# Performance work log

Measured on AMD Instinct MI355X. Metric: run time of the kernel, lower is better.

Reference implementation:

```python
import jax, jax.numpy as jnp
import numpy as np

EPS = 1e-5

def _layernorm(x, w, b):
    mu = jnp.mean(x, axis=-1, keepdims=True)
    var = jnp.mean(jnp.square(x - mu), axis=-1, keepdims=True)
    return (x - mu) * jax.lax.rsqrt(var + EPS) * w + b

def setup_inputs() -> dict:
    key = jax.random.key(0)
    ks = jax.random.split(key, 8)
    B, N, C, D = 32, 1024, 4096, 64
    x = jax.random.normal(ks[0], (B, N, C), dtype=jnp.float32)
    gumbel = jax.random.gumbel(ks[1], (B, N, 2), dtype=jnp.float32)
    ln_w = jnp.ones((C,), jnp.float32)
    ln_b = jnp.zeros((C,), jnp.float32)
    w1 = jax.random.normal(ks[2], (C, D), dtype=jnp.float32) * 0.02
    b1 = jnp.zeros((D,), jnp.float32)
    w2 = jax.random.normal(ks[3], (D, 2), dtype=jnp.float32) * 0.02
    b2 = jnp.zeros((2,), jnp.float32)
    return {"x": x, "gumbel": gumbel, "ln_w": ln_w, "ln_b": ln_b,
            "w1": w1, "b1": b1, "w2": w2, "b2": b2}

def reference(x, gumbel, ln_w, ln_b, w1, b1, w2, b2):
    B, N, C = x.shape
    xn = _layernorm(x, ln_w, ln_b)
    local_x = xn[:, :, : C // 2]                      # [B, N, C/2]
    # policy is all-ones -> weighted mean over tokens
    global_x = jnp.mean(xn[:, :, C // 2:], axis=1, keepdims=True)  # [B, 1, C/2]
    feat = jnp.concatenate(
        [local_x, jnp.broadcast_to(global_x, local_x.shape)], axis=-1)  # [B, N, C]
    h = jax.nn.gelu(feat @ w1 + b1, approximate=False)  # [B, N, 64]
    logits = h @ w2 + b2                                # [B, N, 2]
    pred_score = jax.nn.log_softmax(logits, axis=-1)
    # gumbel-softmax (tau=1, hard=True) with straight-through estimator
    y_soft = jax.nn.softmax(pred_score + gumbel, axis=-1)
    hard = jax.nn.one_hot(jnp.argmax(y_soft, axis=-1), 2, dtype=y_soft.dtype)
    y = hard - jax.lax.stop_gradient(y_soft) + y_soft
    keep = y[:, :, 0]                                   # [B, N]
    # dense equivalent of masked_select/split: zero out dropped tokens
    return x * keep[:, :, None]
```

## Files before the change

kernel.cpp:

```cpp
#include <hip/hip_runtime.h>
#include <math.h>

#define B_   32
#define N_   1024
#define C_   4096
#define HC_  2048
#define D_   64
#define NT_  32768
#define BKC_ 128
#define NCH_ (HC_ / BKC_)
#define AST_ 68

__device__ __forceinline__ float4 ld4(const float* p) {
    return *reinterpret_cast<const float4*>(p);
}

__global__ __launch_bounds__(256) void mk1(
        const float* __restrict__ x, const float* __restrict__ lnw,
        const float* __restrict__ lnb, const float* __restrict__ w1,
        float* __restrict__ Pp, float* __restrict__ muv,
        float* __restrict__ rsv, float* __restrict__ part) {
    __shared__ float smem[16896];
    __shared__ float sLow[64], qLow[64];
    float* As = smem;
    float* Bsm = smem + 8704;

    const int t = threadIdx.x;
    const int tid = blockIdx.x;
    const int T0 = tid * 64;
    const int row = t >> 2;
    const int fq = t & 3;
    const int lane = t & 63, w = t >> 6;
    const int rt = lane >> 3, dt = lane & 7;

    float acc[64];
#pragma unroll
    for (int i = 0; i < 64; ++i) acc[i] = 0.f;
    float sR = 0.f, qR = 0.f;

    float4 xv[8];
    float4 wv[8];
    float lw[8];
    {
        const float* rp = x + (size_t)(T0 + row) * C_ + fq * 32;
#pragma unroll
        for (int i = 0; i < 8; ++i) xv[i] = ld4(rp + i * 4);
        const float4* s4 = reinterpret_cast<const float4*>(w1);
#pragma unroll
        for (int i = 0; i < 8; ++i) {
            wv[i] = s4[i * 256 + t];
            lw[i] = lnw[(i * 256 + t) >> 4];
        }
    }

#pragma unroll 1
    for (int c = 0; c < NCH_; ++c) {
#pragma unroll
        for (int i = 0; i < 8; ++i) {
            const float4 v = xv[i];
            const int kl = fq * 32 + i * 4;
            As[(kl + 0) * AST_ + row] = v.x;
            As[(kl + 1) * AST_ + row] = v.y;
            As[(kl + 2) * AST_ + row] = v.z;
            As[(kl + 3) * AST_ + row] = v.w;
            sR += (v.x + v.y) + (v.z + v.w);
            qR = fmaf(v.x, v.x, fmaf(v.y, v.y,
                 fmaf(v.z, v.z, fmaf(v.w, v.w, qR))));
        }
        {
            float4* b4 = reinterpret_cast<float4*>(Bsm);
#pragma unroll
            for (int i = 0; i < 8; ++i) {
                float4 v = wv[i];
                v.x *= lw[i]; v.y *= lw[i]; v.z *= lw[i]; v.w *= lw[i];
                b4[i * 256 + t] = v;
            }
        }
        __syncthreads();
        if (c + 1 < NCH_) {
            const int k1 = (c + 1) * BKC_;
            const float* rp = x + (size_t)(T0 + row) * C_ + k1 + fq * 32;
#pragma unroll
            for (int i = 0; i < 8; ++i) xv[i] = ld4(rp + i * 4);
            const float4* s4 = reinterpret_cast<const float4*>(
                w1 + (size_t)k1 * D_);
#pragma unroll
            for (int i = 0; i < 8; ++i) {
                wv[i] = s4[i * 256 + t];
                lw[i] = lnw[k1 + ((i * 256 + t) >> 4)];
            }
        }
#pragma unroll 8
        for (int kk = 0; kk < 32; ++kk) {
            const int k = w * 32 + kk;
            const float4 a0 = *reinterpret_cast<const float4*>(
                As + k * AST_ + rt * 8);
            const float4 a1 = *reinterpret_cast<const float4*>(
                As + k * AST_ + rt * 8 + 4);
            const float4 b0 = *reinterpret_cast<const float4*>(
                Bsm + k * 64 + dt * 8);
            const float4 b1 = *reinterpret_cast<const float4*>(
                Bsm + k * 64 + dt * 8 + 4);
            const float av[8] = {a0.x, a0.y, a0.z, a0.w,
                                 a1.x, a1.y, a1.z, a1.w};
            const float bv[8] = {b0.x, b0.y, b0.z, b0.w,
                                 b1.x, b1.y, b1.z, b1.w};
#pragma unroll
            for (int ri = 0; ri < 8; ++ri)
#pragma unroll
                for (int cj = 0; cj < 8; ++cj)
                    acc[ri * 8 + cj] =
                        fmaf(av[ri], bv[cj], acc[ri * 8 + cj]);
        }
        __syncthreads();
    }
    sR += __shfl_xor(sR, 1); qR += __shfl_xor(qR, 1);
    sR += __shfl_xor(sR, 2); qR += __shfl_xor(qR, 2);
    if (fq == 0) { sLow[row] = sR; qLow[row] = qR; }

#pragma unroll
    for (int i = 0; i < 64; ++i) smem[i * 256 + t] = acc[i];
    __syncthreads();
#pragma unroll
    for (int r2 = 0; r2 < 2; ++r2) {
        const int rowO = rt * 8 + w * 2 + r2;
        float v[8];
#pragma unroll
        for (int cj = 0; cj < 8; ++cj) {
            const int i = w * 16 + r2 * 8 + cj;
            v[cj] = (smem[i * 256 + lane]
                     + smem[i * 256 + 64 + lane])
                  + (smem[i * 256 + 128 + lane]
                     + smem[i * 256 + 192 + lane]);
        }
        float* dst = Pp + (size_t)(T0 + rowO) * D_ + dt * 8;
        *reinterpret_cast<float4*>(dst) =
            make_float4(v[0], v[1], v[2], v[3]);
        *reinterpret_cast<float4*>(dst + 4) =
            make_float4(v[4], v[5], v[6], v[7]);
    }
    __syncthreads();

    float4 wvu[8], bvu[8], gacc[8];
#pragma unroll
    for (int m = 0; m < 8; ++m) {
        wvu[m] = ld4(lnw + HC_ + (m * 64 + lane) * 4);
        bvu[m] = ld4(lnb + HC_ + (m * 64 + lane) * 4);
        gacc[m] = make_float4(0.f, 0.f, 0.f, 0.f);
    }
    for (int i = 0; i < 16; ++i) {
        const int r = w * 16 + i;
        const int tok = T0 + r;
        const float* rowp = x + (size_t)tok * C_ + HC_;
        float4 v[8];
        float s = 0.f, q = 0.f;
#pragma unroll
        for (int m = 0; m < 8; ++m) {
            v[m] = ld4(rowp + (m * 64 + lane) * 4);
            s += (v[m].x + v[m].y) + (v[m].z + v[m].w);
            q = fmaf(v[m].x, v[m].x, fmaf(v[m].y, v[m].y,
                fmaf(v[m].z, v[m].z, fmaf(v[m].w, v[m].w, q))));
        }
#pragma unroll
        for (int o = 1; o < 64; o <<= 1) {
            s += __shfl_xor(s, o);
            q += __shfl_xor(q, o);
        }
        const float S_ = s + sLow[r];
        const float Q_ = q + qLow[r];
        const float mu = S_ * (1.f / C_);
        const float rs = rsqrtf(Q_ * (1.f / C_) - mu * mu + 1e-5f);
        if (lane == 0) {
            muv[tok] = mu;
            rsv[tok] = rs;
        }
#pragma unroll
        for (int m = 0; m < 8; ++m) {
            gacc[m].x += (v[m].x - mu) * rs * wvu[m].x + bvu[m].x;
            gacc[m].y += (v[m].y - mu) * rs * wvu[m].y + bvu[m].y;
            gacc[m].z += (v[m].z - mu) * rs * wvu[m].z + bvu[m].z;
            gacc[m].w += (v[m].w - mu) * rs * wvu[m].w + bvu[m].w;
        }
    }
    float (*sh)[HC_] = reinterpret_cast<float(*)[HC_]>(smem);
    __syncthreads();
#pragma unroll
    for (int m = 0; m < 8; ++m)
        *reinterpret_cast<float4*>(&sh[w][(m * 64 + lane) * 4]) = gacc[m];
    __syncthreads();
    float* pp = part + (size_t)tid * HC_;
#pragma unroll
    for (int m = 0; m < 8; ++m) {
        const int j = (m * 64 + lane) * 4;
        const float4 a0 = ld4(&sh[0][j]);
        const float4 a1 = ld4(&sh[1][j]);
        const float4 a2 = ld4(&sh[2][j]);
        const float4 a3 = ld4(&sh[3][j]);
        float4 r;
        r.x = (a0.x + a1.x) + (a2.x + a3.x);
        r.y = (a0.y + a1.y) + (a2.y + a3.y);
        r.z = (a0.z + a1.z) + (a2.z + a3.z);
        r.w = (a0.w + a1.w) + (a2.w + a3.w);
        if (w == (m & 3))
            *reinterpret_cast<float4*>(pp + j) = r;
    }
}

__global__ __launch_bounds__(256) void k2a_part(
        const float* __restrict__ part, const float* __restrict__ w1,
        const float* __restrict__ lnw, const float* __restrict__ lnb,
        float* __restrict__ gpart, float* __restrict__ Wpart,
        float* __restrict__ Bpart) {
    __shared__ float Gs[256];
    __shared__ float red[512];
    const int t = threadIdx.x;
    const int d = t & 63, s = t >> 6;
    const int blk = blockIdx.x;
    if (blk < 256) {
        const int b = blk >> 3, jq = blk & 7;
        const int j = jq * 256 + t;
        float a = 0.f;
        for (int k = 0; k < 16; ++k)
            a += part[(size_t)(b * 16 + k) * HC_ + j];
        Gs[t] = a;
        __syncthreads();
        float acc = 0.f;
        const int j0 = jq * 256 + s * 64;
        for (int jj = 0; jj < 64; ++jj)
            acc = fmaf(Gs[s * 64 + jj],
                       w1[(size_t)(HC_ + j0 + jj) * D_ + d], acc);
        red[s * 64 + d] = acc;
        __syncthreads();
        if (s == 0)
            gpart[(size_t)blk * 64 + d] =
                red[d] + red[64 + d] + red[128 + d] + red[192 + d];
    } else {
        const int wq = blk - 256;
        const int c0 = wq * 256 + s * 64;
        float a = 0.f, c2 = 0.f;
        for (int c = c0; c < c0 + 64; ++c) {
            const float wvv = w1[(size_t)c * D_ + d];
            a = fmaf(lnw[c], wvv, a);
            c2 = fmaf(lnb[c], wvv, c2);
        }
        red[s * 64 + d] = a;
        red[256 + s * 64 + d] = c2;
        __syncthreads();
        if (s == 0) {
            Wpart[wq * 64 + d] =
                red[d] + red[64 + d] + red[128 + d] + red[192 + d];
            Bpart[wq * 64 + d] = red[256 + d] + red[320 + d]
                               + red[384 + d] + red[448 + d];
        }
    }
}

__global__ __launch_bounds__(256) void k45_decide_mask(
        const float* __restrict__ Pp, const float* __restrict__ muv,
        const float* __restrict__ rsv, const float* __restrict__ gpart,
        const float* __restrict__ Wpart, const float* __restrict__ Bpart,
        const float* __restrict__ b1, const float* __restrict__ w2,
        const float* __restrict__ b2, const float* __restrict__ gum,
        const float* __restrict__ x, float* __restrict__ out) {
    const int t = threadIdx.x;
    const int lane = t & 63, w = t >> 6;
    const int token = blockIdx.x * 4 + w;
    const int b = token >> 10;

    float W1 = 0.f, Bsv = 0.f, gt = 0.f;
#pragma unroll
    for (int q = 0; q < 8; ++q) {
        W1 += Wpart[q * 64 + lane];
        Bsv += Bpart[q * 64 + lane];
        gt += gpart[(size_t)(b * 8 + q) * 64 + lane];
    }
    gt *= (1.f / N_);

    const float2 gv = *reinterpret_cast<const float2*>(gum + token * 2);
    const float p = Pp[(size_t)token * D_ + lane];
    const float mu = muv[token], rs = rsv[token];
    float h = rs * (p - mu * W1) + Bsv + gt + b1[lane];
    h = 0.5f * h * (1.f + erff(h * 0.70710678118654752f));
    const float2 w2v = *reinterpret_cast<const float2*>(w2 + lane * 2);
    float l0 = h * w2v.x;
    float l1 = h * w2v.y;
#pragma unroll
    for (int o = 1; o < 64; o <<= 1) {
        l0 += __shfl_xor(l0, o);
        l1 += __shfl_xor(l1, o);
    }
    const float z0 = l0 + b2[0] + gv.x;
    const float z1 = l1 + b2[1] + gv.y;

    float4* dst = reinterpret_cast<float4*>(out + (size_t)token * C_);
    if (z0 >= z1) {
        const float4* src =
            reinterpret_cast<const float4*>(x + (size_t)token * C_);
#pragma unroll
        for (int c = 0; c < 16; ++c)
            dst[c * 64 + lane] = src[c * 64 + lane];
    } else {
        const float4 z = make_float4(0.f, 0.f, 0.f, 0.f);
#pragma unroll
        for (int c = 0; c < 16; ++c)
            dst[c * 64 + lane] = z;
    }
}

extern "C" void kernel_launch(void* const* d_in, const int* in_sizes, int n_in,
                              void* d_out, int out_size, void* d_ws,
                              size_t ws_size, hipStream_t stream) {
    const float* x   = (const float*)d_in[0];
    const float* gum = (const float*)d_in[1];
    const float* lnw = (const float*)d_in[2];
    const float* lnb = (const float*)d_in[3];
    const float* w1  = (const float*)d_in[4];
    const float* b1  = (const float*)d_in[5];
    const float* w2  = (const float*)d_in[6];
    const float* b2  = (const float*)d_in[7];
    float* out = (float*)d_out;

    float* wsf   = (float*)d_ws;
    float* Pp    = wsf;
    float* muv   = Pp + (size_t)NT_ * D_;
    float* rsv   = muv + NT_;
    float* part  = rsv + NT_;
    float* gpart = part + (size_t)512 * HC_;
    float* Wpart = gpart + 256 * 64;
    float* Bpart = Wpart + 8 * 64;

    mk1<<<512, 256, 0, stream>>>(x, lnw, lnb, w1, Pp, muv, rsv, part);
    k2a_part<<<264, 256, 0, stream>>>(part, w1, lnw, lnb,
                                      gpart, Wpart, Bpart);
    k45_decide_mask<<<NT_ / 4, 256, 0, stream>>>(Pp, muv, rsv, gpart,
                                                 Wpart, Bpart, b1, w2, b2,
                                                 gum, x, out);
}
```

Before: 352.6 us.

## Prescale W1 by LN weight in prep kernel and stream it via global_load_lds

Adds a small prep kernel that multiplies w1 by the layernorm weight once and writes it to workspace. The main GEMM kernel then loads each W chunk directly into LDS with global_load_lds DMA instead of staging it through registers with a per-chunk scale. This frees registers and removes the per-block rescaling, but adds a kernel launch. The W load is no longer prefetched into registers one chunk ahead; it is issued at the start of each iteration, before the same barrier that publishes the A tile.

```diff
diff --git a/kernel.cpp b/kernel.cpp
--- a/kernel.cpp
+++ b/kernel.cpp
@@ -15,9 +15,24 @@
     return *reinterpret_cast<const float4*>(p);
 }
 
+#define GLDS16(g, l)                                                        \
+    __builtin_amdgcn_global_load_lds(                                       \
+        (const __attribute__((address_space(1))) unsigned int*)(g),         \
+        (__attribute__((address_space(3))) unsigned int*)(l), 16, 0, 0)
+
+__global__ __launch_bounds__(256) void k0w_prep(
+        const float* __restrict__ lnw, const float* __restrict__ w1,
+        float* __restrict__ wf) {
+    const int idx = blockIdx.x * 256 + threadIdx.x;
+    float4 v = reinterpret_cast<const float4*>(w1)[idx];
+    const float s = lnw[idx >> 4];
+    v.x *= s; v.y *= s; v.z *= s; v.w *= s;
+    reinterpret_cast<float4*>(wf)[idx] = v;
+}
+
 __global__ __launch_bounds__(256) void mk1(
         const float* __restrict__ x, const float* __restrict__ lnw,
-        const float* __restrict__ lnb, const float* __restrict__ w1,
+        const float* __restrict__ lnb, const float* __restrict__ wf,
         float* __restrict__ Pp, float* __restrict__ muv,
         float* __restrict__ rsv, float* __restrict__ part) {
     __shared__ float smem[16896];
@@ -39,22 +54,21 @@
     float sR = 0.f, qR = 0.f;
 
     float4 xv[8];
-    float4 wv[8];
-    float lw[8];
     {
         const float* rp = x + (size_t)(T0 + row) * C_ + fq * 32;
 #pragma unroll
         for (int i = 0; i < 8; ++i) xv[i] = ld4(rp + i * 4);
-        const float4* s4 = reinterpret_cast<const float4*>(w1);
-#pragma unroll
-        for (int i = 0; i < 8; ++i) {
-            wv[i] = s4[i * 256 + t];
-            lw[i] = lnw[(i * 256 + t) >> 4];
-        }
     }
 
 #pragma unroll 1
     for (int c = 0; c < NCH_; ++c) {
+        {
+            const float* wsrc = wf + (size_t)c * BKC_ * D_;
+#pragma unroll
+            for (int i = 0; i < 8; ++i)
+                GLDS16(wsrc + (i * 256 + w * 64 + lane) * 4,
+                       Bsm + i * 1024 + w * 256);
+        }
 #pragma unroll
         for (int i = 0; i < 8; ++i) {
             const float4 v = xv[i];
@@ -67,28 +81,12 @@
             qR = fmaf(v.x, v.x, fmaf(v.y, v.y,
                  fmaf(v.z, v.z, fmaf(v.w, v.w, qR))));
         }
-        {
-            float4* b4 = reinterpret_cast<float4*>(Bsm);
-#pragma unroll
-            for (int i = 0; i < 8; ++i) {
-                float4 v = wv[i];
-                v.x *= lw[i]; v.y *= lw[i]; v.z *= lw[i]; v.w *= lw[i];
-                b4[i * 256 + t] = v;
-            }
-        }
         __syncthreads();
         if (c + 1 < NCH_) {
             const int k1 = (c + 1) * BKC_;
             const float* rp = x + (size_t)(T0 + row) * C_ + k1 + fq * 32;
 #pragma unroll
             for (int i = 0; i < 8; ++i) xv[i] = ld4(rp + i * 4);
-            const float4* s4 = reinterpret_cast<const float4*>(
-                w1 + (size_t)k1 * D_);
-#pragma unroll
-            for (int i = 0; i < 8; ++i) {
-                wv[i] = s4[i * 256 + t];
-                lw[i] = lnw[k1 + ((i * 256 + t) >> 4)];
-            }
         }
 #pragma unroll 8
         for (int kk = 0; kk < 32; ++kk) {
@@ -328,8 +326,10 @@
     float* gpart = part + (size_t)512 * HC_;
     float* Wpart = gpart + 256 * 64;
     float* Bpart = Wpart + 8 * 64;
-
-    mk1<<<512, 256, 0, stream>>>(x, lnw, lnb, w1, Pp, muv, rsv, part);
+    float* wf    = Bpart + 8 * 64;
+
+    k0w_prep<<<128, 256, 0, stream>>>(lnw, w1, wf);
+    mk1<<<512, 256, 0, stream>>>(x, lnw, lnb, wf, Pp, muv, rsv, part);
     k2a_part<<<264, 256, 0, stream>>>(part, w1, lnw, lnb,
                                       gpart, Wpart, Bpart);
     k45_decide_mask<<<NT_ / 4, 256, 0, stream>>>(Pp, muv, rsv, gpart,
```

Result: no change. 355.0 us (+0.7%).
